# Kernel optimization log

Measured on AMD Instinct MI355X. Metric: run time of the kernel, lower is better.

## Reference

```python
import jax, jax.numpy as jnp
import numpy as np

CUBIC_A = -0.75  # torch bicubic kernel coefficient


def _cubic(d):
    a = CUBIC_A
    ad = jnp.abs(d)
    near = (a + 2.0) * ad**3 - (a + 3.0) * ad**2 + 1.0
    far = a * (ad**3 - 5.0 * ad**2 + 8.0 * ad - 4.0)
    return jnp.where(ad <= 1.0, near, jnp.where(ad < 2.0, far, 0.0))


def _axis_weights(in_size, out_size):
    # half-pixel centers (align_corners=False), 4-tap cubic, edge clamp (matches torch)
    scale = in_size / out_size
    src = (jnp.arange(out_size, dtype=jnp.float32) + 0.5) * scale - 0.5
    i0 = jnp.floor(src).astype(jnp.int32)
    offs = jnp.arange(-1, 3)
    taps = i0[:, None] + offs[None, :]          # (out, 4)
    idx = jnp.clip(taps, 0, in_size - 1)
    w = _cubic(src[:, None] - taps.astype(jnp.float32))
    return idx, w


def _bicubic(img, h, w):
    # img: (H, W, C) -> (h, w, C), separable bicubic
    H, W, _ = img.shape
    ih, wh = _axis_weights(H, h)
    iw, ww = _axis_weights(W, w)
    rows = jnp.einsum('ot,otwc->owc', wh, img[ih])   # (h, W, C)
    out = jnp.einsum('ot,hotc->hoc', ww, rows[:, iw])  # (h, w, C)
    return out


def _sincos_1d(embed_dim, t_size):
    omega = np.arange(embed_dim // 2, dtype=np.float32) / (embed_dim / 2.0)
    omega = 1.0 / 10000 ** omega
    out = np.einsum('m,d->md', np.arange(t_size, dtype=np.float32), omega)
    return np.concatenate([np.sin(out), np.cos(out)], axis=1)


HEIGHT, WIDTH, NUM_FRAMES, DIM = 64, 64, 16, 1024
GRIDS = [(8, 32, 32), (8, 48, 48), (4, 64, 64), (1, 64, 64)]


def setup_inputs() -> dict:
    key = jax.random.key(0)
    k1, k2 = jax.random.split(key)
    total = sum(t * h * w for t, h, w in GRIDS)  # 47104
    x = jax.random.normal(k1, (total, DIM), dtype=jnp.float32)
    weight = jax.random.normal(k2, (HEIGHT, WIDTH, DIM), dtype=jnp.float32) * 0.02
    time_weight = jnp.asarray(_sincos_1d(DIM, NUM_FRAMES))[:, None, :]  # (T, 1, dim)
    grid_thws = jnp.asarray(GRIDS, dtype=jnp.int64)
    return {"x": x, "weight": weight, "time_weight": time_weight, "grid_thws": grid_thws}


def reference(x, weight, time_weight, grid_thws):
    H, W, dim = weight.shape
    grids = np.asarray(grid_thws).tolist()  # static per-sample shapes
    pos_embs = []
    for t, h, w in grids:
        if (h, w) == (H, W):
            pe2 = weight.reshape(-1, dim)
        else:
            pe2 = _bicubic(weight, h, w).reshape(-1, dim)
        if t == 1:
            pe3 = pe2
        else:
            pe3 = pe2[None, :, :] + time_weight[:t]  # (t, h*w, dim)
        pos_embs.append(pe3.reshape(-1, dim))
    return x + jnp.concatenate(pos_embs, axis=0)
```

## Files before the change

### kernel.cpp

```cpp
#include <hip/hip_runtime.h>

#define CUBIC_A (-0.75f)

typedef float f4nt __attribute__((ext_vector_type(4)));

__device__ __forceinline__ void nt_store4(float4* p, float4 v) {
    f4nt t;
    t.x = v.x; t.y = v.y; t.z = v.z; t.w = v.w;
    __builtin_nontemporal_store(t, (f4nt*)p);
}

__device__ __forceinline__ float4 add3(float4 a, float4 b, float4 c) {
    return make_float4(a.x + b.x + c.x, a.y + b.y + c.y,
                       a.z + b.z + c.z, a.w + b.w + c.w);
}
__device__ __forceinline__ float4 add2(float4 a, float4 b) {
    return make_float4(a.x + b.x, a.y + b.y, a.z + b.z, a.w + b.w);
}

__device__ __forceinline__ float cubic_w(float d) {
    float ad = fabsf(d);
    if (ad <= 1.0f) return ((CUBIC_A + 2.0f) * ad - (CUBIC_A + 3.0f)) * ad * ad + 1.0f;
    if (ad < 2.0f)  return CUBIC_A * (((ad - 5.0f) * ad + 8.0f) * ad - 4.0f);
    return 0.0f;
}

__device__ __forceinline__ float4 bicubic_pe(const float4* __restrict__ wgt,
                                             int px, int out_hw, int d4) {
    const int i = px / out_hw;
    const int j = px % out_hw;
    const float scale = 64.0f / (float)out_hw;
    const float si = ((float)i + 0.5f) * scale - 0.5f;
    const float sj = ((float)j + 0.5f) * scale - 0.5f;
    const int i0 = (int)floorf(si);
    const int j0 = (int)floorf(sj);
    int ih[4], iw[4];
    float wh[4], ww[4];
#pragma unroll
    for (int a = 0; a < 4; ++a) {
        int tp = i0 - 1 + a;
        wh[a] = cubic_w(si - (float)tp);
        ih[a] = min(63, max(0, tp));
        tp = j0 - 1 + a;
        ww[a] = cubic_w(sj - (float)tp);
        iw[a] = min(63, max(0, tp));
    }
    float ax = 0.f, ay = 0.f, az = 0.f, aw = 0.f;
#pragma unroll
    for (int a = 0; a < 4; ++a) {
        float rx = 0.f, ry = 0.f, rz = 0.f, rw = 0.f;
#pragma unroll
        for (int c = 0; c < 4; ++c) {
            const float4 v = wgt[(size_t)(ih[a] * 64 + iw[c]) * 256 + d4];
            rx = fmaf(ww[c], v.x, rx);
            ry = fmaf(ww[c], v.y, ry);
            rz = fmaf(ww[c], v.z, rz);
            rw = fmaf(ww[c], v.w, rw);
        }
        ax = fmaf(wh[a], rx, ax);
        ay = fmaf(wh[a], ry, ay);
        az = fmaf(wh[a], rz, az);
        aw = fmaf(wh[a], rw, aw);
    }
    return make_float4(ax, ay, az, aw);
}

__global__ __launch_bounds__(512) void posemb_kernel(
    const float4* __restrict__ x,
    const float4* __restrict__ wgt,
    const float4* __restrict__ tw,
    float4* __restrict__ out)
{
    const int b   = blockIdx.x;
    const int tid = threadIdx.x;
    const int d4  = tid & 255;
    const int fh  = tid >> 8;

    if (b < 1024) {
        const int px = b;
        const size_t base = ((size_t)(fh * 1024 + px)) * 256 + d4;
        const size_t st   = (size_t)2048 * 256;
        const float4 xv0 = x[base];
        const float4 xv1 = x[base + st];
        const float4 xv2 = x[base + 2 * st];
        const float4 xv3 = x[base + 3 * st];
        const float4 tv0 = tw[(size_t)(fh    ) * 256 + d4];
        const float4 tv1 = tw[(size_t)(fh + 2) * 256 + d4];
        const float4 tv2 = tw[(size_t)(fh + 4) * 256 + d4];
        const float4 tv3 = tw[(size_t)(fh + 6) * 256 + d4];
        const float4 pe = bicubic_pe(wgt, px, 32, d4);
        nt_store4(&out[base],          add3(xv0, pe, tv0));
        nt_store4(&out[base + st],     add3(xv1, pe, tv1));
        nt_store4(&out[base + 2 * st], add3(xv2, pe, tv2));
        nt_store4(&out[base + 3 * st], add3(xv3, pe, tv3));
    } else if (b < 3328) {
        const int px = b - 1024;
        const size_t base = ((size_t)(8192 + fh * 2304 + px)) * 256 + d4;
        const size_t st   = (size_t)2 * 2304 * 256;
        const float4 xv0 = x[base];
        const float4 xv1 = x[base + st];
        const float4 xv2 = x[base + 2 * st];
        const float4 xv3 = x[base + 3 * st];
        const float4 tv0 = tw[(size_t)(fh    ) * 256 + d4];
        const float4 tv1 = tw[(size_t)(fh + 2) * 256 + d4];
        const float4 tv2 = tw[(size_t)(fh + 4) * 256 + d4];
        const float4 tv3 = tw[(size_t)(fh + 6) * 256 + d4];
        const float4 pe = bicubic_pe(wgt, px, 48, d4);
        nt_store4(&out[base],          add3(xv0, pe, tv0));
        nt_store4(&out[base + st],     add3(xv1, pe, tv1));
        nt_store4(&out[base + 2 * st], add3(xv2, pe, tv2));
        nt_store4(&out[base + 3 * st], add3(xv3, pe, tv3));
    } else if (b < 7424) {
        const int px = b - 3328;
        const size_t base = ((size_t)(26624 + fh * 4096 + px)) * 256 + d4;
        const size_t st   = (size_t)2 * 4096 * 256;
        const float4 xv0 = x[base];
        const float4 xv1 = x[base + st];
        const float4 pe  = wgt[(size_t)px * 256 + d4];
        const float4 tv0 = tw[(size_t)(fh    ) * 256 + d4];
        const float4 tv1 = tw[(size_t)(fh + 2) * 256 + d4];
        nt_store4(&out[base],      add3(xv0, pe, tv0));
        nt_store4(&out[base + st], add3(xv1, pe, tv1));
    } else {
        const int px = 2 * (b - 7424) + fh;
        const size_t e = ((size_t)(43008 + px)) * 256 + d4;
        const float4 xv = x[e];
        const float4 pe = wgt[(size_t)px * 256 + d4];
        nt_store4(&out[e], add2(xv, pe));
    }
}

extern "C" void kernel_launch(void* const* d_in, const int* in_sizes, int n_in,
                              void* d_out, int out_size, void* d_ws, size_t ws_size,
                              hipStream_t stream) {
    const float4* x   = (const float4*)d_in[0];
    const float4* wgt = (const float4*)d_in[1];
    const float4* tw  = (const float4*)d_in[2];
    float4* out = (float4*)d_out;
    posemb_kernel<<<9472, 512, 0, stream>>>(x, wgt, tw, out);
}
```

Before: 76.72 us.

## Precompute bicubic position embeddings into workspace before the add pass

Splits the fused kernel into a pre-pass that computes the interpolated 32x32 and 48x48 position embeddings once into the workspace, and a streaming add kernel that reads them. This removes the redundant 16-tap gather and weight arithmetic done per frame-half in every block. The cost is an extra launch plus a write and reread of about 13MB of intermediate data in a bandwidth-bound kernel. The original fused kernel is kept as a fallback for when the workspace is too small.

Result: slower. 83.00 us (+8.2%).

```diff
diff --git a/kernel.cpp b/kernel.cpp
--- a/kernel.cpp
+++ b/kernel.cpp
@@ -65,10 +65,23 @@
     return make_float4(ax, ay, az, aw);
 }
 
-__global__ __launch_bounds__(512) void posemb_kernel(
+__global__ __launch_bounds__(256) void pe_build_kernel(
+    const float4* __restrict__ wgt,
+    float4* __restrict__ pe_ws)
+{
+    const int b  = blockIdx.x;
+    const int d4 = threadIdx.x;
+    float4 pe;
+    if (b < 1024) pe = bicubic_pe(wgt, b, 32, d4);
+    else          pe = bicubic_pe(wgt, b - 1024, 48, d4);
+    pe_ws[(size_t)b * 256 + d4] = pe;
+}
+
+__global__ __launch_bounds__(512) void posemb_add_kernel(
     const float4* __restrict__ x,
     const float4* __restrict__ wgt,
     const float4* __restrict__ tw,
+    const float4* __restrict__ pe_ws,
     float4* __restrict__ out)
 {
     const int b   = blockIdx.x;
@@ -84,11 +97,11 @@
         const float4 xv1 = x[base + st];
         const float4 xv2 = x[base + 2 * st];
         const float4 xv3 = x[base + 3 * st];
-        const float4 tv0 = tw[(size_t)(fh    ) * 256 + d4];
-        const float4 tv1 = tw[(size_t)(fh + 2) * 256 + d4];
-        const float4 tv2 = tw[(size_t)(fh + 4) * 256 + d4];
-        const float4 tv3 = tw[(size_t)(fh + 6) * 256 + d4];
-        const float4 pe = bicubic_pe(wgt, px, 32, d4);
+        const float4 pe  = pe_ws[(size_t)px * 256 + d4];
+        const float4 tv0 = tw[(size_t)(fh    ) * 256 + d4];
+        const float4 tv1 = tw[(size_t)(fh + 2) * 256 + d4];
+        const float4 tv2 = tw[(size_t)(fh + 4) * 256 + d4];
+        const float4 tv3 = tw[(size_t)(fh + 6) * 256 + d4];
         nt_store4(&out[base],          add3(xv0, pe, tv0));
         nt_store4(&out[base + st],     add3(xv1, pe, tv1));
         nt_store4(&out[base + 2 * st], add3(xv2, pe, tv2));
@@ -101,11 +114,11 @@
         const float4 xv1 = x[base + st];
         const float4 xv2 = x[base + 2 * st];
         const float4 xv3 = x[base + 3 * st];
-        const float4 tv0 = tw[(size_t)(fh    ) * 256 + d4];
-        const float4 tv1 = tw[(size_t)(fh + 2) * 256 + d4];
-        const float4 tv2 = tw[(size_t)(fh + 4) * 256 + d4];
-        const float4 tv3 = tw[(size_t)(fh + 6) * 256 + d4];
-        const float4 pe = bicubic_pe(wgt, px, 48, d4);
+        const float4 pe  = pe_ws[(size_t)(1024 + px) * 256 + d4];
+        const float4 tv0 = tw[(size_t)(fh    ) * 256 + d4];
+        const float4 tv1 = tw[(size_t)(fh + 2) * 256 + d4];
+        const float4 tv2 = tw[(size_t)(fh + 4) * 256 + d4];
+        const float4 tv3 = tw[(size_t)(fh + 6) * 256 + d4];
         nt_store4(&out[base],          add3(xv0, pe, tv0));
         nt_store4(&out[base + st],     add3(xv1, pe, tv1));
         nt_store4(&out[base + 2 * st], add3(xv2, pe, tv2));
@@ -130,6 +143,69 @@
     }
 }
 
+__global__ __launch_bounds__(512) void posemb_fallback_kernel(
+    const float4* __restrict__ x, const float4* __restrict__ wgt,
+    const float4* __restrict__ tw, float4* __restrict__ out)
+{
+    const int b   = blockIdx.x;
+    const int tid = threadIdx.x;
+    const int d4  = tid & 255;
+    const int fh  = tid >> 8;
+
+    if (b < 1024) {
+        const int px = b;
+        const size_t base = ((size_t)(fh * 1024 + px)) * 256 + d4;
+        const size_t st   = (size_t)2048 * 256;
+        const float4 xv0 = x[base];
+        const float4 xv1 = x[base + st];
+        const float4 xv2 = x[base + 2 * st];
+        const float4 xv3 = x[base + 3 * st];
+        const float4 tv0 = tw[(size_t)(fh    ) * 256 + d4];
+        const float4 tv1 = tw[(size_t)(fh + 2) * 256 + d4];
+        const float4 tv2 = tw[(size_t)(fh + 4) * 256 + d4];
+        const float4 tv3 = tw[(size_t)(fh + 6) * 256 + d4];
+        const float4 pe = bicubic_pe(wgt, px, 32, d4);
+        nt_store4(&out[base],          add3(xv0, pe, tv0));
+        nt_store4(&out[base + st],     add3(xv1, pe, tv1));
+        nt_store4(&out[base + 2 * st], add3(xv2, pe, tv2));
+        nt_store4(&out[base + 3 * st], add3(xv3, pe, tv3));
+    } else if (b < 3328) {
+        const int px = b - 1024;
+        const size_t base = ((size_t)(8192 + fh * 2304 + px)) * 256 + d4;
+        const size_t st   = (size_t)2 * 2304 * 256;
+        const float4 xv0 = x[base];
+        const float4 xv1 = x[base + st];
+        const float4 xv2 = x[base + 2 * st];
+        const float4 xv3 = x[base + 3 * st];
+        const float4 tv0 = tw[(size_t)(fh    ) * 256 + d4];
+        const float4 tv1 = tw[(size_t)(fh + 2) * 256 + d4];
+        const float4 tv2 = tw[(size_t)(fh + 4) * 256 + d4];
+        const float4 tv3 = tw[(size_t)(fh + 6) * 256 + d4];
+        const float4 pe = bicubic_pe(wgt, px, 48, d4);
+        nt_store4(&out[base],          add3(xv0, pe, tv0));
+        nt_store4(&out[base + st],     add3(xv1, pe, tv1));
+        nt_store4(&out[base + 2 * st], add3(xv2, pe, tv2));
+        nt_store4(&out[base + 3 * st], add3(xv3, pe, tv3));
+    } else if (b < 7424) {
+        const int px = b - 3328;
+        const size_t base = ((size_t)(26624 + fh * 4096 + px)) * 256 + d4;
+        const size_t st   = (size_t)2 * 4096 * 256;
+        const float4 xv0 = x[base];
+        const float4 xv1 = x[base + st];
+        const float4 pe  = wgt[(size_t)px * 256 + d4];
+        const float4 tv0 = tw[(size_t)(fh    ) * 256 + d4];
+        const float4 tv1 = tw[(size_t)(fh + 2) * 256 + d4];
+        nt_store4(&out[base],      add3(xv0, pe, tv0));
+        nt_store4(&out[base + st], add3(xv1, pe, tv1));
+    } else {
+        const int px = 2 * (b - 7424) + fh;
+        const size_t e = ((size_t)(43008 + px)) * 256 + d4;
+        const float4 xv = x[e];
+        const float4 pe = wgt[(size_t)px * 256 + d4];
+        nt_store4(&out[e], add2(xv, pe));
+    }
+}
+
 extern "C" void kernel_launch(void* const* d_in, const int* in_sizes, int n_in,
                               void* d_out, int out_size, void* d_ws, size_t ws_size,
                               hipStream_t stream) {
@@ -137,5 +213,13 @@
     const float4* wgt = (const float4*)d_in[1];
     const float4* tw  = (const float4*)d_in[2];
     float4* out = (float4*)d_out;
-    posemb_kernel<<<9472, 512, 0, stream>>>(x, wgt, tw, out);
-}
+
+    const size_t pe_bytes = (size_t)3328 * 256 * sizeof(float4);
+    if (ws_size >= pe_bytes) {
+        float4* pe_ws = (float4*)d_ws;
+        pe_build_kernel<<<3328, 256, 0, stream>>>(wgt, pe_ws);
+        posemb_add_kernel<<<9472, 512, 0, stream>>>(x, wgt, tw, pe_ws, out);
+    } else {
+        posemb_fallback_kernel<<<9472, 512, 0, stream>>>(x, wgt, tw, out);
+    }
+}
```

## Process all frames per pixel in one 256-thread block to avoid duplicate bicubic

Applied to the files above, without the earlier changes.

Each block now covers one spatial pixel across all its frames with 256 threads, instead of two frame-halves in 512 threads. As a result the bicubic interpolation, with its 16 gathered weight loads, is computed once per pixel rather than twice. Each thread issues more independent loads and stores (up to eight frames). The trade-off is more registers per thread and fewer waves overall.

Result: no change. 77.24 us (+0.7%).

```diff
diff --git a/kernel.cpp b/kernel.cpp
--- a/kernel.cpp
+++ b/kernel.cpp
@@ -65,68 +65,100 @@
     return make_float4(ax, ay, az, aw);
 }
 
-__global__ __launch_bounds__(512) void posemb_kernel(
+__global__ __launch_bounds__(256, 2) void posemb_kernel(
     const float4* __restrict__ x,
     const float4* __restrict__ wgt,
     const float4* __restrict__ tw,
     float4* __restrict__ out)
 {
-    const int b   = blockIdx.x;
-    const int tid = threadIdx.x;
-    const int d4  = tid & 255;
-    const int fh  = tid >> 8;
+    const int b  = blockIdx.x;
+    const int d4 = threadIdx.x;
 
     if (b < 1024) {
         const int px = b;
-        const size_t base = ((size_t)(fh * 1024 + px)) * 256 + d4;
-        const size_t st   = (size_t)2048 * 256;
+        const size_t base = (size_t)px * 256 + d4;
+        const size_t st   = (size_t)1024 * 256;
         const float4 xv0 = x[base];
         const float4 xv1 = x[base + st];
         const float4 xv2 = x[base + 2 * st];
         const float4 xv3 = x[base + 3 * st];
-        const float4 tv0 = tw[(size_t)(fh    ) * 256 + d4];
-        const float4 tv1 = tw[(size_t)(fh + 2) * 256 + d4];
-        const float4 tv2 = tw[(size_t)(fh + 4) * 256 + d4];
-        const float4 tv3 = tw[(size_t)(fh + 6) * 256 + d4];
+        const float4 xv4 = x[base + 4 * st];
+        const float4 xv5 = x[base + 5 * st];
+        const float4 xv6 = x[base + 6 * st];
+        const float4 xv7 = x[base + 7 * st];
+        const float4 tv0 = tw[(size_t)0 * 256 + d4];
+        const float4 tv1 = tw[(size_t)1 * 256 + d4];
+        const float4 tv2 = tw[(size_t)2 * 256 + d4];
+        const float4 tv3 = tw[(size_t)3 * 256 + d4];
+        const float4 tv4 = tw[(size_t)4 * 256 + d4];
+        const float4 tv5 = tw[(size_t)5 * 256 + d4];
+        const float4 tv6 = tw[(size_t)6 * 256 + d4];
+        const float4 tv7 = tw[(size_t)7 * 256 + d4];
         const float4 pe = bicubic_pe(wgt, px, 32, d4);
         nt_store4(&out[base],          add3(xv0, pe, tv0));
         nt_store4(&out[base + st],     add3(xv1, pe, tv1));
         nt_store4(&out[base + 2 * st], add3(xv2, pe, tv2));
         nt_store4(&out[base + 3 * st], add3(xv3, pe, tv3));
+        nt_store4(&out[base + 4 * st], add3(xv4, pe, tv4));
+        nt_store4(&out[base + 5 * st], add3(xv5, pe, tv5));
+        nt_store4(&out[base + 6 * st], add3(xv6, pe, tv6));
+        nt_store4(&out[base + 7 * st], add3(xv7, pe, tv7));
     } else if (b < 3328) {
         const int px = b - 1024;
-        const size_t base = ((size_t)(8192 + fh * 2304 + px)) * 256 + d4;
-        const size_t st   = (size_t)2 * 2304 * 256;
+        const size_t base = (size_t)(8192 + px) * 256 + d4;
+        const size_t st   = (size_t)2304 * 256;
         const float4 xv0 = x[base];
         const float4 xv1 = x[base + st];
         const float4 xv2 = x[base + 2 * st];
         const float4 xv3 = x[base + 3 * st];
-        const float4 tv0 = tw[(size_t)(fh    ) * 256 + d4];
-        const float4 tv1 = tw[(size_t)(fh + 2) * 256 + d4];
-        const float4 tv2 = tw[(size_t)(fh + 4) * 256 + d4];
-        const float4 tv3 = tw[(size_t)(fh + 6) * 256 + d4];
+        const float4 xv4 = x[base + 4 * st];
+        const float4 xv5 = x[base + 5 * st];
+        const float4 xv6 = x[base + 6 * st];
+        const float4 xv7 = x[base + 7 * st];
+        const float4 tv0 = tw[(size_t)0 * 256 + d4];
+        const float4 tv1 = tw[(size_t)1 * 256 + d4];
+        const float4 tv2 = tw[(size_t)2 * 256 + d4];
+        const float4 tv3 = tw[(size_t)3 * 256 + d4];
+        const float4 tv4 = tw[(size_t)4 * 256 + d4];
+        const float4 tv5 = tw[(size_t)5 * 256 + d4];
+        const float4 tv6 = tw[(size_t)6 * 256 + d4];
+        const float4 tv7 = tw[(size_t)7 * 256 + d4];
         const float4 pe = bicubic_pe(wgt, px, 48, d4);
         nt_store4(&out[base],          add3(xv0, pe, tv0));
         nt_store4(&out[base + st],     add3(xv1, pe, tv1));
         nt_store4(&out[base + 2 * st], add3(xv2, pe, tv2));
         nt_store4(&out[base + 3 * st], add3(xv3, pe, tv3));
+        nt_store4(&out[base + 4 * st], add3(xv4, pe, tv4));
+        nt_store4(&out[base + 5 * st], add3(xv5, pe, tv5));
+        nt_store4(&out[base + 6 * st], add3(xv6, pe, tv6));
+        nt_store4(&out[base + 7 * st], add3(xv7, pe, tv7));
     } else if (b < 7424) {
         const int px = b - 3328;
-        const size_t base = ((size_t)(26624 + fh * 4096 + px)) * 256 + d4;
-        const size_t st   = (size_t)2 * 4096 * 256;
+        const size_t base = (size_t)(26624 + px) * 256 + d4;
+        const size_t st   = (size_t)4096 * 256;
         const float4 xv0 = x[base];
         const float4 xv1 = x[base + st];
+        const float4 xv2 = x[base + 2 * st];
+        const float4 xv3 = x[base + 3 * st];
+        const float4 tv0 = tw[(size_t)0 * 256 + d4];
+        const float4 tv1 = tw[(size_t)1 * 256 + d4];
+        const float4 tv2 = tw[(size_t)2 * 256 + d4];
+        const float4 tv3 = tw[(size_t)3 * 256 + d4];
         const float4 pe  = wgt[(size_t)px * 256 + d4];
-        const float4 tv0 = tw[(size_t)(fh    ) * 256 + d4];
-        const float4 tv1 = tw[(size_t)(fh + 2) * 256 + d4];
-        nt_store4(&out[base],      add3(xv0, pe, tv0));
-        nt_store4(&out[base + st], add3(xv1, pe, tv1));
+        nt_store4(&out[base],          add3(xv0, pe, tv0));
+        nt_store4(&out[base + st],     add3(xv1, pe, tv1));
+        nt_store4(&out[base + 2 * st], add3(xv2, pe, tv2));
+        nt_store4(&out[base + 3 * st], add3(xv3, pe, tv3));
     } else {
-        const int px = 2 * (b - 7424) + fh;
-        const size_t e = ((size_t)(43008 + px)) * 256 + d4;
-        const float4 xv = x[e];
-        const float4 pe = wgt[(size_t)px * 256 + d4];
-        nt_store4(&out[e], add2(xv, pe));
+        const int px0 = 2 * (b - 7424);
+        const size_t e0 = (size_t)(43008 + px0) * 256 + d4;
+        const size_t e1 = e0 + 256;
+        const float4 xv0 = x[e0];
+        const float4 xv1 = x[e1];
+        const float4 pe0 = wgt[(size_t)px0 * 256 + d4];
+        const float4 pe1 = wgt[(size_t)(px0 + 1) * 256 + d4];
+        nt_store4(&out[e0], add2(xv0, pe0));
+        nt_store4(&out[e1], add2(xv1, pe1));
     }
 }
 
@@ -137,5 +169,5 @@
     const float4* wgt = (const float4*)d_in[1];
     const float4* tw  = (const float4*)d_in[2];
     float4* out = (float4*)d_out;
-    posemb_kernel<<<9472, 512, 0, stream>>>(x, wgt, tw, out);
+    posemb_kernel<<<9472, 256, 0, stream>>>(x, wgt, tw, out);
 }
```
